# Kernel tuning notes

Hardware: AMD Instinct MI355X
Metric: run time of the kernel (lower is better)

Reference implementation:

```python
import jax, jax.numpy as jnp
import numpy as np

C_CURV = 1.0          # Poincare ball curvature
EPS = 1e-5
MAX_NORM = (1.0 - 1e-4) / np.sqrt(C_CURV)


def _artanh(x):
    x = jnp.clip(x, -1.0 + 1e-5, 1.0 - 1e-5)
    return 0.5 * (jnp.log1p(x) - jnp.log1p(-x))


def _expmap0(v):
    # v: [N,C,H,W]; norm over channel dim per spatial location
    n = jnp.maximum(jnp.linalg.norm(v, axis=1, keepdims=True), EPS)
    sc = np.sqrt(C_CURV)
    return jnp.tanh(sc * n) * v / (sc * n)


def _logmap0(y):
    n = jnp.maximum(jnp.linalg.norm(y, axis=1, keepdims=True), EPS)
    sc = np.sqrt(C_CURV)
    return _artanh(sc * n) * y / (sc * n)


def _project(y):
    # clamp back inside the ball
    n = jnp.maximum(jnp.linalg.norm(y, axis=1, keepdims=True), EPS)
    return jnp.where(n > MAX_NORM, y * (MAX_NORM / n), y)


def _conv3x3(u, w, b):
    y = jax.lax.conv_general_dilated(u, w, window_strides=(1, 1),
                                     padding=((1, 1), (1, 1)),
                                     dimension_numbers=('NCHW', 'OIHW', 'NCHW'))
    return y + b[None, :, None, None]


def _hconv(x, w, b):
    # HConvolution2d: tangent-space conv around origin
    return _project(_expmap0(_conv3x3(_logmap0(x), w, b)))


def _hbn(x, gamma, beta):
    # HBatchNorm2d: Euclidean BN in the tangent space at the origin (training stats)
    u = _logmap0(x)
    m = u.mean(axis=(0, 2, 3), keepdims=True)
    v = u.var(axis=(0, 2, 3), keepdims=True)
    u = (u - m) / jnp.sqrt(v + 1e-5)
    u = u * gamma[None, :, None, None] + beta[None, :, None, None]
    return _project(_expmap0(u))


def _hrelu(x):
    return _project(_expmap0(jax.nn.relu(_logmap0(x))))


def setup_inputs() -> dict:
    key = jax.random.key(0)
    ks = jax.random.split(key, 8)
    N, Cin, Cmid, Cout, H, W = 8, 32, 32, 32, 256, 256
    # input point on the Poincare ball
    x = _project(_expmap0(0.1 * jax.random.normal(ks[0], (N, Cin, H, W), jnp.float32)))
    fan1 = Cin * 9
    fan2 = Cmid * 9
    w1 = jax.random.normal(ks[1], (Cmid, Cin, 3, 3), jnp.float32) / np.sqrt(fan1)
    b1 = jnp.zeros((Cmid,), jnp.float32)
    g1 = jnp.ones((Cmid,), jnp.float32)
    beta1 = jnp.zeros((Cmid,), jnp.float32)
    w2 = jax.random.normal(ks[2], (Cout, Cmid, 3, 3), jnp.float32) / np.sqrt(fan2)
    b2 = jnp.zeros((Cout,), jnp.float32)
    g2 = jnp.ones((Cout,), jnp.float32)
    beta2 = jnp.zeros((Cout,), jnp.float32)
    return {"x": x, "w1": w1, "b1": b1, "g1": g1, "beta1": beta1,
            "w2": w2, "b2": b2, "g2": g2, "beta2": beta2}


def reference(x, w1, b1, g1, beta1, w2, b2, g2, beta2):
    out = _hconv(x, w1, b1)
    out = _hbn(out, g1, beta1)
    out = _hrelu(out)
    out = _hconv(out, w2, b2)
    out = _hbn(out, g2, beta2)
    out = _hrelu(out)
    return out
```

## Files before the change

### kernel.cpp

```cpp
#include <hip/hip_runtime.h>
#include <math.h>

#define HWDIM 256
#define CH 32
#define NB 8
#define TILE 16
#define NLOC (NB*HWDIM*HWDIM)
#define R_CLAMP 4.9517189f
#define MAXN 0.9999f
#define BN_EPS 1e-5f
#define EPSF 1e-5f
#define NBLK 2048
#define OST 264

typedef __attribute__((ext_vector_type(8))) _Float16 half8;
typedef __attribute__((ext_vector_type(4))) float floatx4;

__device__ __forceinline__ float artanh_c(float n) {
    float t = fminf(n, 1.0f - 1e-5f);
    return 0.5f * (log1pf(t) - log1pf(-t));
}

__global__ __launch_bounds__(256) void wprep_kernel(
    const float* __restrict__ w1, const float* __restrict__ w2,
    _Float16* __restrict__ wp1, _Float16* __restrict__ wp2)
{
    int idx = blockIdx.x * 256 + threadIdx.x;
    if (idx >= 2*CH*CH*9) return;
    int s = idx >= CH*CH*9;
    int id = idx - s*(CH*CH*9);
    const float* w = s ? w2 : w1;
    _Float16* wp = s ? wp2 : wp1;
    int j  = id & 7;
    int r  = id >> 3;
    int co = r & 31;
    int og = r >> 5;
    int g  = og & 3;
    int o  = og >> 2;
    int ci = g*8 + j;
    wp[id] = (_Float16)w[(co*CH + ci)*9 + o];
}

template<int STAGE>
__global__ __launch_bounds__(256) void conv_mfma_kernel(
    const void* __restrict__ srcv,
    const _Float16* __restrict__ wp,
    const float* __restrict__ bias,
    const float* __restrict__ scsh,
    _Float16* __restrict__ dst,
    float* __restrict__ partials)
{
    __shared__ _Float16 ah[10368];
    __shared__ float red[4][64];

    const int tid = threadIdx.x;
    const int bx = blockIdx.x, by = blockIdx.y, bz = blockIdx.z;
    const int h0 = by*TILE - 1, w0 = bx*TILE - 1;

    for (int loc = tid; loc < 324; loc += 256) {
        int y = loc / 18, x = loc - y*18;
        int gh = h0 + y, gw = w0 + x;
        if (gh < 0 || gh >= HWDIM || gw < 0 || gw >= HWDIM) {
            half8 z = {0,0,0,0,0,0,0,0};
            #pragma unroll
            for (int g = 0; g < 4; g++) *(half8*)(ah + ((y*4+g)*18 + x)*8) = z;
            continue;
        }
        float v[CH]; float n2 = 0.f;
        if (STAGE == 1) {
            const float* p = (const float*)srcv + ((size_t)bz*CH << 16) + gh*HWDIM + gw;
            #pragma unroll
            for (int c = 0; c < CH; c++) { float t = p[(size_t)c << 16]; v[c] = t; n2 = fmaf(t, t, n2); }
            float n = fmaxf(sqrtf(n2), EPSF);
            float f = artanh_c(n) / n;
            #pragma unroll
            for (int c = 0; c < CH; c++) v[c] *= f;
        } else {
            const _Float16* p = (const _Float16*)srcv + (((size_t)bz << 16) + gh*HWDIM + gw)*CH;
            half8 raw[4];
            #pragma unroll
            for (int k = 0; k < 4; k++) raw[k] = *(const half8*)(p + 8*k);
            #pragma unroll
            for (int c = 0; c < CH; c++) {
                float t = fmaf((float)raw[c>>3][c&7], scsh[c], scsh[CH + c]);
                v[c] = t; n2 = fmaf(t, t, n2);
            }
            float n = sqrtf(n2);
            float f = (n > R_CLAMP) ? (R_CLAMP / n) : 1.0f;
            #pragma unroll
            for (int c = 0; c < CH; c++) v[c] = fmaxf(v[c]*f, 0.0f);
        }
        #pragma unroll
        for (int g = 0; g < 4; g++) {
            half8 hv;
            #pragma unroll
            for (int j = 0; j < 8; j++) hv[j] = (_Float16)v[g*8 + j];
            *(half8*)(ah + ((y*4+g)*18 + x)*8) = hv;
        }
    }
    __syncthreads();

    const int lane = tid & 63, wave = tid >> 6;
    const int xx = lane & 15, q = lane >> 4;

    floatx4 acc[4][2];
    #pragma unroll
    for (int i = 0; i < 4; i++) {
        acc[i][0] = (floatx4){0.f,0.f,0.f,0.f};
        acc[i][1] = (floatx4){0.f,0.f,0.f,0.f};
    }

    #pragma unroll
    for (int dx = 0; dx < 3; dx++) {
        half8 af[6];
        #pragma unroll
        for (int yy = 0; yy < 6; yy++)
            af[yy] = *(const half8*)(ah + (((wave*4+yy)*4 + q)*18 + xx + dx)*8);
        #pragma unroll
        for (int dy = 0; dy < 3; dy++) {
            const int o = dy*3 + dx;
            const _Float16* wb = wp + (size_t)((o*4 + q)*32)*8;
            half8 b0 = *(const half8*)(wb + xx*8);
            half8 b1 = *(const half8*)(wb + (xx+16)*8);
            #pragma unroll
            for (int i = 0; i < 4; i++) {
                acc[i][0] = __builtin_amdgcn_mfma_f32_16x16x32_f16(af[i+dy], b0, acc[i][0], 0,0,0);
                acc[i][1] = __builtin_amdgcn_mfma_f32_16x16x32_f16(af[i+dy], b1, acc[i][1], 0,0,0);
            }
        }
    }

    {
        float b0 = bias[xx], b1 = bias[xx + 16];
        #pragma unroll
        for (int i = 0; i < 4; i++)
            #pragma unroll
            for (int r = 0; r < 4; r++) { acc[i][0][r] += b0; acc[i][1][r] += b1; }

        #pragma unroll
        for (int i = 0; i < 4; i++) {
            #pragma unroll
            for (int r = 0; r < 4; r++) {
                float n2 = acc[i][0][r]*acc[i][0][r] + acc[i][1][r]*acc[i][1][r];
                n2 += __shfl_xor(n2, 1, 64);
                n2 += __shfl_xor(n2, 2, 64);
                n2 += __shfl_xor(n2, 4, 64);
                n2 += __shfl_xor(n2, 8, 64);
                float nn = sqrtf(n2);
                float f = (nn > R_CLAMP) ? (R_CLAMP/nn) : 1.0f;
                acc[i][0][r] *= f; acc[i][1][r] *= f;
            }
        }
        float s0=0.f, q0=0.f, s1=0.f, q1=0.f;
        #pragma unroll
        for (int i = 0; i < 4; i++)
            #pragma unroll
            for (int r = 0; r < 4; r++) {
                float a0 = acc[i][0][r], a1 = acc[i][1][r];
                s0 += a0; q0 = fmaf(a0, a0, q0);
                s1 += a1; q1 = fmaf(a1, a1, q1);
            }
        s0 += __shfl_xor(s0, 16, 64); s0 += __shfl_xor(s0, 32, 64);
        q0 += __shfl_xor(q0, 16, 64); q0 += __shfl_xor(q0, 32, 64);
        s1 += __shfl_xor(s1, 16, 64); s1 += __shfl_xor(s1, 32, 64);
        q1 += __shfl_xor(q1, 16, 64); q1 += __shfl_xor(q1, 32, 64);
        if (q == 0) {
            red[wave][xx]      = s0;
            red[wave][16 + xx] = s1;
            red[wave][32 + xx] = q0;
            red[wave][48 + xx] = q1;
        }
    }

    {
        _Float16* dp = dst + (((size_t)bz << 16) + (size_t)(by*TILE)*HWDIM + bx*TILE)*CH;
        #pragma unroll
        for (int i = 0; i < 4; i++) {
            int yl = wave*4 + i;
            #pragma unroll
            for (int r = 0; r < 4; r++) {
                int xl = q*4 + r;
                _Float16* a = dp + ((size_t)yl*HWDIM + xl)*CH;
                a[xx]      = (_Float16)acc[i][0][r];
                a[xx + 16] = (_Float16)acc[i][1][r];
            }
        }
    }
    __syncthreads();
    if (tid < 64) {
        float s = red[0][tid] + red[1][tid] + red[2][tid] + red[3][tid];
        int bid = (bz*gridDim.y + by)*gridDim.x + bx;
        partials[(size_t)tid*NBLK + bid] = s;
    }
}

__global__ __launch_bounds__(256) void finalize_kernel(
    const float* __restrict__ partials,
    const float* __restrict__ g, const float* __restrict__ beta,
    float* __restrict__ scsh)
{
    __shared__ float ss[256], sq[256];
    const int c = blockIdx.x;
    const int tid = threadIdx.x;
    float s = 0.f, q = 0.f;
    for (int b = tid; b < NBLK; b += 256) {
        s += partials[(size_t)c*NBLK + b];
        q += partials[(size_t)(CH + c)*NBLK + b];
    }
    ss[tid] = s; sq[tid] = q;
    __syncthreads();
    for (int st = 128; st > 0; st >>= 1) {
        if (tid < st) { ss[tid] += ss[tid+st]; sq[tid] += sq[tid+st]; }
        __syncthreads();
    }
    if (tid == 0) {
        const float NS = (float)NLOC;
        float mean = ss[0] / NS;
        float var = fmaxf(sq[0] / NS - mean*mean, 0.0f);
        float sc = g[c] / sqrtf(var + BN_EPS);
        scsh[c] = sc;
        scsh[CH + c] = beta[c] - mean*sc;
    }
}

__global__ __launch_bounds__(256) void out_kernel(
    const _Float16* __restrict__ t4c, const float* __restrict__ scsh,
    float* __restrict__ out)
{
    __shared__ float outb[16*OST];
    const int w = threadIdx.x;
    const int h = blockIdx.x, n = blockIdx.y;
    const _Float16* p = t4c + (((size_t)n << 16) + (size_t)h*HWDIM + w)*CH;
    half8 raw[4];
    #pragma unroll
    for (int k = 0; k < 4; k++) raw[k] = *(const half8*)(p + 8*k);
    float u[CH]; float n2 = 0.f;
    #pragma unroll
    for (int c = 0; c < CH; c++) {
        float t = fmaf((float)raw[c>>3][c&7], scsh[c], scsh[CH+c]);
        u[c] = t; n2 = fmaf(t, t, n2);
    }
    float nn = sqrtf(n2);
    float f = (nn > R_CLAMP) ? (R_CLAMP/nn) : 1.0f;
    float r2 = 0.f;
    #pragma unroll
    for (int c = 0; c < CH; c++) { float r = fmaxf(u[c]*f, 0.0f); u[c] = r; r2 = fmaf(r, r, r2); }
    float rn = fmaxf(sqrtf(r2), EPSF);
    float s = fminf(tanhf(rn), MAXN) / rn;
    #pragma unroll
    for (int c = 0; c < CH; c++) u[c] *= s;

    #pragma unroll
    for (int hf = 0; hf < 2; hf++) {
        if (hf) __syncthreads();
        #pragma unroll
        for (int c = 0; c < 16; c++) outb[c*OST + w] = u[hf*16 + c];
        __syncthreads();
        int co = threadIdx.x >> 4, seg = threadIdx.x & 15;
        const float* row = outb + co*OST + seg*16;
        float* gp = out + ((size_t)(n*CH + hf*16 + co) << 16) + (size_t)h*HWDIM + seg*16;
        #pragma unroll
        for (int k = 0; k < 4; k++) *(floatx4*)(gp + 4*k) = *(const floatx4*)(row + 4*k);
    }
}

extern "C" void kernel_launch(void* const* d_in, const int* in_sizes, int n_in,
                              void* d_out, int out_size, void* d_ws, size_t ws_size,
                              hipStream_t stream)
{
    const float* x   = (const float*)d_in[0];
    const float* w1  = (const float*)d_in[1];
    const float* b1  = (const float*)d_in[2];
    const float* g1  = (const float*)d_in[3];
    const float* be1 = (const float*)d_in[4];
    const float* w2  = (const float*)d_in[5];
    const float* b2  = (const float*)d_in[6];
    const float* g2  = (const float*)d_in[7];
    const float* be2 = (const float*)d_in[8];
    float* outf = (float*)d_out;

    char* ws = (char*)d_ws;
    _Float16* wp1   = (_Float16*)ws;
    _Float16* wp2   = wp1 + 9216;
    float* partials = (float*)(ws + 36864);
    float* scsh1    = (float*)(ws + 36864 + 524288);
    float* scsh2    = scsh1 + 64;
    _Float16* t1c   = (_Float16*)(scsh2 + 64);
    _Float16* t4c   = t1c + (size_t)NLOC*CH;

    wprep_kernel<<<72, 256, 0, stream>>>(w1, w2, wp1, wp2);

    dim3 grid(HWDIM/TILE, HWDIM/TILE, NB);

    conv_mfma_kernel<1><<<grid, 256, 0, stream>>>(x, wp1, b1, scsh1, t1c, partials);
    finalize_kernel<<<32, 256, 0, stream>>>(partials, g1, be1, scsh1);
    conv_mfma_kernel<2><<<grid, 256, 0, stream>>>(t1c, wp2, b2, scsh1, t4c, partials);
    finalize_kernel<<<32, 256, 0, stream>>>(partials, g2, be2, scsh2);
    out_kernel<<<dim3(HWDIM, NB), 256, 0, stream>>>(t4c, scsh2, outf);
}
```

Measured before the change: 226.8 us.

## Transpose MFMA operands for channel-major accumulators and vectorized fp16 stores

Swaps the A/B operands of the MFMA so each lane holds four consecutive output channels for one pixel instead of four pixels for one channel. Epilogue stores become half4 vector writes instead of scalar fp16 writes, and the per-pixel norm reduction needs only two cross-lane shuffles. The channel statistics now need more shuffles. The grid is also flattened to 1D with batch in the low bits, so consecutive blocks cover different images at the same spatial tile, which changes cache locality.

```diff
diff --git a/kernel.cpp b/kernel.cpp
--- a/kernel.cpp
+++ b/kernel.cpp
@@ -14,6 +14,7 @@
 #define OST 264
 
 typedef __attribute__((ext_vector_type(8))) _Float16 half8;
+typedef __attribute__((ext_vector_type(4))) _Float16 half4;
 typedef __attribute__((ext_vector_type(4))) float floatx4;
 
 __device__ __forceinline__ float artanh_c(float n) {
@@ -54,7 +55,10 @@
     __shared__ float red[4][64];
 
     const int tid = threadIdx.x;
-    const int bx = blockIdx.x, by = blockIdx.y, bz = blockIdx.z;
+    const int flat = blockIdx.x;
+    const int bz = flat & 7;
+    const int t  = flat >> 3;
+    const int by = t >> 4, bx = t & 15;
     const int h0 = by*TILE - 1, w0 = bx*TILE - 1;
 
     for (int loc = tid; loc < 324; loc += 256) {
@@ -70,7 +74,7 @@
         if (STAGE == 1) {
             const float* p = (const float*)srcv + ((size_t)bz*CH << 16) + gh*HWDIM + gw;
             #pragma unroll
-            for (int c = 0; c < CH; c++) { float t = p[(size_t)c << 16]; v[c] = t; n2 = fmaf(t, t, n2); }
+            for (int c = 0; c < CH; c++) { float t0 = p[(size_t)c << 16]; v[c] = t0; n2 = fmaf(t0, t0, n2); }
             float n = fmaxf(sqrtf(n2), EPSF);
             float f = artanh_c(n) / n;
             #pragma unroll
@@ -82,8 +86,8 @@
             for (int k = 0; k < 4; k++) raw[k] = *(const half8*)(p + 8*k);
             #pragma unroll
             for (int c = 0; c < CH; c++) {
-                float t = fmaf((float)raw[c>>3][c&7], scsh[c], scsh[CH + c]);
-                v[c] = t; n2 = fmaf(t, t, n2);
+                float t0 = fmaf((float)raw[c>>3][c&7], scsh[c], scsh[CH + c]);
+                v[c] = t0; n2 = fmaf(t0, t0, n2);
             }
             float n = sqrtf(n2);
             float f = (n > R_CLAMP) ? (R_CLAMP / n) : 1.0f;
@@ -120,77 +124,74 @@
         for (int dy = 0; dy < 3; dy++) {
             const int o = dy*3 + dx;
             const _Float16* wb = wp + (size_t)((o*4 + q)*32)*8;
-            half8 b0 = *(const half8*)(wb + xx*8);
-            half8 b1 = *(const half8*)(wb + (xx+16)*8);
+            half8 wf0 = *(const half8*)(wb + xx*8);
+            half8 wf1 = *(const half8*)(wb + (xx+16)*8);
             #pragma unroll
             for (int i = 0; i < 4; i++) {
-                acc[i][0] = __builtin_amdgcn_mfma_f32_16x16x32_f16(af[i+dy], b0, acc[i][0], 0,0,0);
-                acc[i][1] = __builtin_amdgcn_mfma_f32_16x16x32_f16(af[i+dy], b1, acc[i][1], 0,0,0);
+                acc[i][0] = __builtin_amdgcn_mfma_f32_16x16x32_f16(wf0, af[i+dy], acc[i][0], 0,0,0);
+                acc[i][1] = __builtin_amdgcn_mfma_f32_16x16x32_f16(wf1, af[i+dy], acc[i][1], 0,0,0);
             }
         }
     }
 
-    {
-        float b0 = bias[xx], b1 = bias[xx + 16];
-        #pragma unroll
-        for (int i = 0; i < 4; i++)
-            #pragma unroll
-            for (int r = 0; r < 4; r++) { acc[i][0][r] += b0; acc[i][1][r] += b1; }
-
-        #pragma unroll
-        for (int i = 0; i < 4; i++) {
-            #pragma unroll
-            for (int r = 0; r < 4; r++) {
-                float n2 = acc[i][0][r]*acc[i][0][r] + acc[i][1][r]*acc[i][1][r];
-                n2 += __shfl_xor(n2, 1, 64);
-                n2 += __shfl_xor(n2, 2, 64);
-                n2 += __shfl_xor(n2, 4, 64);
-                n2 += __shfl_xor(n2, 8, 64);
-                float nn = sqrtf(n2);
-                float f = (nn > R_CLAMP) ? (R_CLAMP/nn) : 1.0f;
-                acc[i][0][r] *= f; acc[i][1][r] *= f;
-            }
-        }
-        float s0=0.f, q0=0.f, s1=0.f, q1=0.f;
-        #pragma unroll
-        for (int i = 0; i < 4; i++)
-            #pragma unroll
-            for (int r = 0; r < 4; r++) {
-                float a0 = acc[i][0][r], a1 = acc[i][1][r];
-                s0 += a0; q0 = fmaf(a0, a0, q0);
-                s1 += a1; q1 = fmaf(a1, a1, q1);
-            }
-        s0 += __shfl_xor(s0, 16, 64); s0 += __shfl_xor(s0, 32, 64);
-        q0 += __shfl_xor(q0, 16, 64); q0 += __shfl_xor(q0, 32, 64);
-        s1 += __shfl_xor(s1, 16, 64); s1 += __shfl_xor(s1, 32, 64);
-        q1 += __shfl_xor(q1, 16, 64); q1 += __shfl_xor(q1, 32, 64);
-        if (q == 0) {
-            red[wave][xx]      = s0;
-            red[wave][16 + xx] = s1;
-            red[wave][32 + xx] = q0;
-            red[wave][48 + xx] = q1;
-        }
-    }
-
-    {
-        _Float16* dp = dst + (((size_t)bz << 16) + (size_t)(by*TILE)*HWDIM + bx*TILE)*CH;
-        #pragma unroll
-        for (int i = 0; i < 4; i++) {
-            int yl = wave*4 + i;
-            #pragma unroll
-            for (int r = 0; r < 4; r++) {
-                int xl = q*4 + r;
-                _Float16* a = dp + ((size_t)yl*HWDIM + xl)*CH;
-                a[xx]      = (_Float16)acc[i][0][r];
-                a[xx + 16] = (_Float16)acc[i][1][r];
-            }
+    float bs[8];
+    #pragma unroll
+    for (int r = 0; r < 4; r++) { bs[r] = bias[q*4+r]; bs[4+r] = bias[q*4+r+16]; }
+    float sv[8], qv[8];
+    #pragma unroll
+    for (int k = 0; k < 8; k++) { sv[k] = 0.f; qv[k] = 0.f; }
+
+    _Float16* dp = dst + (((size_t)bz << 16) + (size_t)(by*TILE)*HWDIM + bx*TILE + xx)*CH + q*4;
+
+    #pragma unroll
+    for (int i = 0; i < 4; i++) {
+        float n2 = 0.f;
+        #pragma unroll
+        for (int r = 0; r < 4; r++) {
+            acc[i][0][r] += bs[r];
+            acc[i][1][r] += bs[4+r];
+            n2 = fmaf(acc[i][0][r], acc[i][0][r], n2);
+            n2 = fmaf(acc[i][1][r], acc[i][1][r], n2);
+        }
+        n2 += __shfl_xor(n2, 16, 64);
+        n2 += __shfl_xor(n2, 32, 64);
+        float nn = sqrtf(n2);
+        float f = (nn > R_CLAMP) ? (R_CLAMP/nn) : 1.0f;
+        half4 o0, o1;
+        #pragma unroll
+        for (int r = 0; r < 4; r++) {
+            float a0 = acc[i][0][r] * f;
+            float a1 = acc[i][1][r] * f;
+            sv[r]   += a0; qv[r]   = fmaf(a0, a0, qv[r]);
+            sv[4+r] += a1; qv[4+r] = fmaf(a1, a1, qv[4+r]);
+            o0[r] = (_Float16)a0; o1[r] = (_Float16)a1;
+        }
+        _Float16* a = dp + (size_t)(wave*4 + i)*HWDIM*CH;
+        *(half4*)(a)      = o0;
+        *(half4*)(a + 16) = o1;
+    }
+
+    #pragma unroll
+    for (int k = 0; k < 8; k++) {
+        #pragma unroll
+        for (int m = 1; m < 16; m <<= 1) {
+            sv[k] += __shfl_xor(sv[k], m, 64);
+            qv[k] += __shfl_xor(qv[k], m, 64);
+        }
+    }
+    if (xx == 0) {
+        #pragma unroll
+        for (int r = 0; r < 4; r++) {
+            red[wave][q*4+r]        = sv[r];
+            red[wave][16 + q*4+r]   = sv[4+r];
+            red[wave][32 + q*4+r]   = qv[r];
+            red[wave][48 + q*4+r]   = qv[4+r];
         }
     }
     __syncthreads();
     if (tid < 64) {
         float s = red[0][tid] + red[1][tid] + red[2][tid] + red[3][tid];
-        int bid = (bz*gridDim.y + by)*gridDim.x + bx;
-        partials[(size_t)tid*NBLK + bid] = s;
+        partials[(size_t)tid*NBLK + flat] = s;
     }
 }
 
@@ -290,11 +291,9 @@
 
     wprep_kernel<<<72, 256, 0, stream>>>(w1, w2, wp1, wp2);
 
-    dim3 grid(HWDIM/TILE, HWDIM/TILE, NB);
-
-    conv_mfma_kernel<1><<<grid, 256, 0, stream>>>(x, wp1, b1, scsh1, t1c, partials);
+    conv_mfma_kernel<1><<<NBLK, 256, 0, stream>>>(x, wp1, b1, scsh1, t1c, partials);
     finalize_kernel<<<32, 256, 0, stream>>>(partials, g1, be1, scsh1);
-    conv_mfma_kernel<2><<<grid, 256, 0, stream>>>(t1c, wp2, b2, scsh1, t4c, partials);
+    conv_mfma_kernel<2><<<NBLK, 256, 0, stream>>>(t1c, wp2, b2, scsh1, t4c, partials);
     finalize_kernel<<<32, 256, 0, stream>>>(partials, g2, be2, scsh2);
     out_kernel<<<dim3(HWDIM, NB), 256, 0, stream>>>(t4c, scsh2, outf);
 }
```

Measured after the change: 204.5 us. -9.8%, faster.
